# Optimization experiments

Measured on AMD Instinct MI355X. Metric: run time of the kernel, lower is better.

## Reference

```python
import jax, jax.numpy as jnp
import numpy as np

E, S, L, H, C = 32, 64, 20, 512, 32  # episodes, steps, max_comm_len, hidden_size, comm_shape
STD_MIN, STD_MAX = 2.0611536e-09, 7.389056  # exp(-20), exp(2)


def setup_inputs() -> dict:
    key = jax.random.key(0)
    ks = jax.random.split(key, 12)
    def p(k, shape):
        return jax.random.normal(k, shape, jnp.float32) * 0.02
    return {
        'x': jax.random.normal(ks[0], (E, S, H), jnp.float32),
        'Wr': p(ks[1], (2 * H, H)), 'br': jnp.zeros((H,), jnp.float32),
        'Wz': p(ks[2], (2 * H, H)), 'bz': jnp.zeros((H,), jnp.float32),
        'Wn': p(ks[3], (2 * H, H)), 'bn': jnp.zeros((H,), jnp.float32),
        'conv_w1': p(ks[4], (H // 4, H, 1)), 'conv_b1': jnp.zeros((H // 4,), jnp.float32),
        'conv_w3': p(ks[5], (H // 4, H, 3)), 'conv_b3': jnp.zeros((H // 4,), jnp.float32),
        'conv_w5': p(ks[6], (H // 4, H, 5)), 'conv_b5': jnp.zeros((H // 4,), jnp.float32),
        'conv_w7': p(ks[7], (H // 4, H, 7)), 'conv_b7': jnp.zeros((H // 4,), jnp.float32),
        'prelu_a': jnp.asarray(0.25, jnp.float32),
        'W_mu': p(ks[8], (H, C)), 'b_mu': jnp.zeros((C,), jnp.float32),
        'W_std': p(ks[9], (H, C)), 'b_std': jnp.zeros((C,), jnp.float32),
        'eps': jax.random.normal(ks[10], (E, S, L, C), jnp.float32),
    }


def reference(x, Wr, br, Wz, bz, Wn, bn,
              conv_w1, conv_b1, conv_w3, conv_b3, conv_w5, conv_b5, conv_w7, conv_b7,
              prelu_a, W_mu, b_mu, W_std, b_std, eps):
    B = E * S
    xf = x.reshape(B, H)  # same input fed to the RNN at every comm step

    def step(h, _):
        xh = jnp.concatenate([xf, h], -1)
        r = jax.nn.sigmoid(xh @ Wr + br)
        z = jax.nn.sigmoid(xh @ Wz + bz)
        n = jnp.tanh(jnp.concatenate([xf, r * h], -1) @ Wn + bn)
        h_new = (1.0 - z) * n + z * h  # time_constant=1 -> h = new GRU state
        return h_new, h_new

    h0 = jnp.zeros((B, H), x.dtype)
    _, hs = jax.lax.scan(step, h0, None, length=L)  # (L, B, H)
    comm_h = jnp.transpose(hs, (1, 2, 0))  # (B, H, L) -- NCW layout for conv

    dn = ('NCH', 'OIH', 'NCH')
    def conv(w, b, k):
        pad = (k - 1) // 2
        y = jax.lax.conv_general_dilated(comm_h, w, (1,), [(pad, pad)], dimension_numbers=dn)
        return y + b[None, :, None]

    y = jnp.concatenate([
        conv(conv_w1, conv_b1, 1),
        conv(conv_w3, conv_b3, 3),
        conv(conv_w5, conv_b5, 5),
        conv(conv_w7, conv_b7, 7),
    ], axis=1)  # (B, H, L)
    y = jnp.where(y >= 0, y, prelu_a * y)  # PReLU; dropout is identity in eval
    y = jnp.transpose(y, (0, 2, 1)).reshape(E, S, L, H)

    mu = y @ W_mu + b_mu
    std = jnp.clip(jax.nn.softplus(y @ W_std + b_std), STD_MIN, STD_MAX)
    comm = mu + eps * std  # reparameterized Normal sample
    comm_out = jnp.tanh(comm)
    log2pi = jnp.asarray(np.log(2.0 * np.pi), jnp.float32)
    log_prob = (-0.5 * ((comm - mu) / std) ** 2 - jnp.log(std) - 0.5 * log2pi
                - jnp.log(1.0 - comm_out ** 2 + 1e-6))
    log_prob = jnp.mean(log_prob, -1, keepdims=True)  # (E,S,L,1)
    log_prob = jnp.mean(log_prob, -2)  # (E,S,1)
    return comm_out, log_prob
```

## Files before the change

### kernel.cpp

```cpp
#include <hip/hip_runtime.h>
#include <hip/hip_bf16.h>

typedef __hip_bfloat16 bf16;
typedef short short8 __attribute__((ext_vector_type(8)));
typedef float floatx4 __attribute__((ext_vector_type(4)));

#define BDIM 2048
#define HDIM 512
#define LDIM 20
#define CDIM 32
#define LSTR 40

__device__ __forceinline__ float sigm(float x) { return 1.0f / (1.0f + expf(-x)); }

__device__ __forceinline__ void ll16(const short* g, short* l)
{
    __builtin_amdgcn_global_load_lds(
        (const __attribute__((address_space(1))) void*)g,
        (__attribute__((address_space(3))) void*)l, 16, 0, 0);
}
#define WAITVM(N) asm volatile("s_waitcnt vmcnt(" #N ")" ::: "memory")

__device__ __forceinline__ void gemm_tile_k(
    const short* __restrict__ A, int lda,
    const short* __restrict__ Bt, int ldb,
    int K, short* lds, floatx4 (&acc)[4][4], int tid)
{
    short* As = lds;
    short* Bs = lds + 128 * LSTR;
    const int wave = tid >> 6, lane = tid & 63;
    const int wm = wave & 1, wn = wave >> 1;
    const int m16 = lane & 15, quad = lane >> 4;
    const int r0 = tid >> 2;
    const int koff = (tid & 3) * 8;

    short8 a0 = *(const short8*)(A + (size_t)r0 * lda + koff);
    short8 a1 = *(const short8*)(A + (size_t)(r0 + 64) * lda + koff);
    short8 b0 = *(const short8*)(Bt + (size_t)r0 * ldb + koff);
    short8 b1 = *(const short8*)(Bt + (size_t)(r0 + 64) * ldb + koff);
    for (int k0 = 0; k0 < K; k0 += 32) {
        __syncthreads();
        *(short8*)(As + r0 * LSTR + koff) = a0;
        *(short8*)(As + (r0 + 64) * LSTR + koff) = a1;
        *(short8*)(Bs + r0 * LSTR + koff) = b0;
        *(short8*)(Bs + (r0 + 64) * LSTR + koff) = b1;
        __syncthreads();
        if (k0 + 32 < K) {
            a0 = *(const short8*)(A + (size_t)r0 * lda + k0 + 32 + koff);
            a1 = *(const short8*)(A + (size_t)(r0 + 64) * lda + k0 + 32 + koff);
            b0 = *(const short8*)(Bt + (size_t)r0 * ldb + k0 + 32 + koff);
            b1 = *(const short8*)(Bt + (size_t)(r0 + 64) * ldb + k0 + 32 + koff);
        }
        short8 af[4], bfr[4];
#pragma unroll
        for (int i = 0; i < 4; ++i)
            af[i] = *(short8*)(As + (wm * 64 + i * 16 + m16) * LSTR + quad * 8);
#pragma unroll
        for (int j = 0; j < 4; ++j)
            bfr[j] = *(short8*)(Bs + (wn * 64 + j * 16 + m16) * LSTR + quad * 8);
#pragma unroll
        for (int i = 0; i < 4; ++i)
#pragma unroll
            for (int j = 0; j < 4; ++j)
                acc[i][j] = __builtin_amdgcn_mfma_f32_16x16x32_bf16(
                    af[i], bfr[j], acc[i][j], 0, 0, 0);
    }
}

__global__ __launch_bounds__(256) void k_prep_xb(const float* __restrict__ x,
                                                 bf16* __restrict__ xb)
{
    int i = blockIdx.x * 256 + threadIdx.x;
    xb[i] = (bf16)x[i];
}

__global__ __launch_bounds__(256) void k_transpose_512(const float* __restrict__ src,
                                                       bf16* __restrict__ dst)
{
    __shared__ float tile[32][33];
    int tx = threadIdx.x & 31, ty = threadIdx.x >> 5;
    int k0 = blockIdx.x * 32, n0 = blockIdx.y * 32;
#pragma unroll
    for (int i = 0; i < 32; i += 8)
        tile[ty + i][tx] = src[(size_t)(k0 + ty + i) * 512 + n0 + tx];
    __syncthreads();
#pragma unroll
    for (int i = 0; i < 32; i += 8)
        dst[(size_t)(n0 + ty + i) * 512 + k0 + tx] = (bf16)tile[tx][ty + i];
}

__global__ __launch_bounds__(256) void k_swzW(const float* __restrict__ Wr,
                                              const float* __restrict__ Wz,
                                              const float* __restrict__ Wn,
                                              bf16* __restrict__ Wfrag)
{
    int idx = blockIdx.x * 256 + threadIdx.x;
    int e = idx & 7, lane = (idx >> 3) & 63;
    int t2 = idx >> 9;
    int f = t2 % 6, jk = t2 / 6;
    int kc = jk & 15, j = jk >> 4;
    int ftype = f >> 1;
    int col = j * 32 + (f & 1) * 16 + (lane & 15);
    int k = kc * 32 + ((lane >> 4) << 3) + e;
    const float* W = (ftype == 0) ? Wr : (ftype == 1) ? Wz : Wn;
    Wfrag[idx] = (bf16)W[(size_t)(512 + k) * 512 + col];
}

__global__ __launch_bounds__(256) void k_prep_wc(
    const float* __restrict__ w1, const float* __restrict__ w3,
    const float* __restrict__ w5, const float* __restrict__ w7,
    bf16* __restrict__ wt)
{
    int idx = blockIdx.x * 256 + threadIdx.x;
    int g, base;
    if (idx < 65536)       { g = 0; base = 0;      }
    else if (idx < 262144) { g = 1; base = 65536;  }
    else if (idx < 589824) { g = 2; base = 262144; }
    else                   { g = 3; base = 589824; }
    int rel = idx - base;
    int k = 2 * g + 1;
    int ci = rel & 511;
    int t2 = rel >> 9;
    int co = t2 & 127;
    int tap = t2 >> 7;
    const float* w = (g == 0) ? w1 : (g == 1) ? w3 : (g == 2) ? w5 : w7;
    wt[idx] = (bf16)w[((size_t)co * 512 + ci) * k + tap];
}

__global__ __launch_bounds__(256) void k_prep_wh(const float* __restrict__ Wmu,
                                                 const float* __restrict__ Wstd,
                                                 bf16* __restrict__ Wh_t)
{
    int idx = blockIdx.x * 256 + threadIdx.x;
    int n = idx >> 9, k = idx & 511;
    float v = (n < 32) ? Wmu[(size_t)k * 32 + n] : Wstd[(size_t)k * 32 + (n - 32)];
    Wh_t[idx] = (bf16)v;
}

__global__ __launch_bounds__(256) void k_gx(
    const bf16* __restrict__ xb, const bf16* __restrict__ Wx_t,
    const float* __restrict__ br, const float* __restrict__ bz,
    const float* __restrict__ bn, bf16* __restrict__ gxb)
{
    __shared__ short lds[2 * 128 * LSTR];
    const int tid = threadIdx.x;
    const int row0 = blockIdx.x * 128, col0 = blockIdx.y * 128;
    floatx4 acc[4][4];
#pragma unroll
    for (int i = 0; i < 4; ++i)
#pragma unroll
        for (int j = 0; j < 4; ++j) acc[i][j] = (floatx4)0.0f;
    gemm_tile_k((const short*)xb + (size_t)row0 * 512, 512,
                (const short*)Wx_t + (size_t)col0 * 512, 512, 512, lds, acc, tid);
    const int wave = tid >> 6, lane = tid & 63;
    const int wm = wave & 1, wn = wave >> 1;
    const int m16 = lane & 15, quad = lane >> 4;
#pragma unroll
    for (int i = 0; i < 4; ++i)
#pragma unroll
        for (int j = 0; j < 4; ++j)
#pragma unroll
            for (int reg = 0; reg < 4; ++reg) {
                int b = row0 + wm * 64 + i * 16 + quad * 4 + reg;
                int n = col0 + wn * 64 + j * 16 + m16;
                float bias = (n < 512) ? br[n] : (n < 1024) ? bz[n - 512] : bn[n - 1024];
                gxb[(size_t)b * 1536 + n] = (bf16)(acc[i][j][reg] + bias);
            }
}

__device__ __forceinline__ void gbar(unsigned* c, unsigned target, bool fast)
{
    WAITVM(0);
    __syncthreads();
    if (threadIdx.x == 0) {
        if (!fast) __threadfence();
        __hip_atomic_fetch_add(c, 1u, __ATOMIC_RELAXED, __HIP_MEMORY_SCOPE_AGENT);
        unsigned v = __hip_atomic_load(c, __ATOMIC_RELAXED, __HIP_MEMORY_SCOPE_AGENT);
        int guard = 0;
        while (v < target && ++guard < (1 << 24)) {
            __builtin_amdgcn_s_sleep(1);
            v = __hip_atomic_load(c, __ATOMIC_RELAXED, __HIP_MEMORY_SCOPE_AGENT);
        }
        if (!fast) __threadfence();
        else asm volatile("buffer_inv" ::: "memory");
    }
    __syncthreads();
}

template<int NF>
__device__ __forceinline__ void phase_ring(
    const short* __restrict__ srcw, const short* __restrict__ wl,
    short* ringw, int f0, int lane, floatx4 (&acc)[NF])
{
    const short* g = srcw + (size_t)(lane & 15) * 512 + (lane >> 4) * 8;
#pragma unroll
    for (int p = 0; p < 4; ++p)
        ll16(g + p * 32, ringw + p * 512);
#pragma unroll
    for (int kc = 0; kc < 16; ++kc) {
        if (kc < 13)      { WAITVM(3); }
        else if (kc == 13){ WAITVM(2); }
        else if (kc == 14){ WAITVM(1); }
        else              { WAITVM(0); }
        short8 a = *(short8*)(ringw + (kc & 3) * 512 + lane * 8);
        short8 bfr[NF];
#pragma unroll
        for (int f = 0; f < NF; ++f)
            bfr[f] = *(short8*)(wl + ((kc * 6 + f0 + f) << 9) + lane * 8);
        asm volatile("s_waitcnt lgkmcnt(0)" ::: "memory");
        __builtin_amdgcn_sched_barrier(0);
        if (kc < 12)
            ll16(g + (kc + 4) * 32, ringw + (kc & 3) * 512);
#pragma unroll
        for (int f = 0; f < NF; ++f)
            acc[f] = __builtin_amdgcn_mfma_f32_16x16x32_bf16(a, bfr[f], acc[f], 0, 0, 0);
    }
}

__global__ __launch_bounds__(512, 2) void k_gru8(
    const bf16* __restrict__ Wfrag, const bf16* __restrict__ gxb,
    bf16* __restrict__ hs, bf16* __restrict__ rhb,
    unsigned* __restrict__ ctr, int* __restrict__ xcdtab)
{
    __shared__ short wlds[6 * 16 * 512];
    __shared__ short aring[8 * 4 * 512];
    const int tid = threadIdx.x;
    const int wave = tid >> 6, lane = tid & 63;
    const int m16 = lane & 15, quad = lane >> 4;
    const int b = blockIdx.x;
    const int s = b >> 3;
    const int m = (b & 7) + ((s & 1) << 3);
    const int j = s >> 1;
    const int wrow = wave * 16;
    unsigned* mctr = ctr + m * 32;
    short* ringw = aring + wave * 2048;

    int myxcd;
    asm volatile("s_getreg_b32 %0, hwreg(HW_REG_XCC_ID)" : "=s"(myxcd));
    myxcd &= 15;
    if (tid == 0) xcdtab[m * 16 + j] = myxcd;

    const short* wsrc = (const short*)Wfrag + (size_t)j * 49152;
#pragma unroll
    for (int r = 0; r < 12; ++r)
        ll16(wsrc + ((wave * 12 + r) << 9) + lane * 8, wlds + ((wave * 12 + r) << 9));

    float gxr[2][4], gxz[2][4], gxn[2][4];
#pragma unroll
    for (int reg = 0; reg < 4; ++reg) {
        const bf16* gp = gxb + (size_t)(m * 128 + wrow + quad * 4 + reg) * 1536 + j * 32;
#pragma unroll
        for (int fc = 0; fc < 2; ++fc) {
            int c = fc * 16 + m16;
            gxr[fc][reg] = __bfloat162float(gp[c]);
            gxz[fc][reg] = __bfloat162float(gp[512 + c]);
            gxn[fc][reg] = __bfloat162float(gp[1024 + c]);
        }
    }

    gbar(mctr + 1, 16u, false);
    bool fast = true;
#pragma unroll
    for (int jj = 0; jj < 16; ++jj)
        fast = fast && (xcdtab[m * 16 + jj] == myxcd);

    float h32[2][4] = {};
    float zf[2][4];
    unsigned nbar = 0;
    const int rowg = m * 128 + wrow + quad * 4;

    for (int t = 0; t < LDIM; ++t) {
        floatx4 acc[4];
#pragma unroll
        for (int f = 0; f < 4; ++f) acc[f] = (floatx4)0.0f;
        if (t > 0)
            phase_ring<4>((const short*)hs + ((size_t)(t - 1) * BDIM + m * 128 + wrow) * 512,
                          wlds, ringw, 0, lane, acc);
#pragma unroll
        for (int fc = 0; fc < 2; ++fc)
#pragma unroll
            for (int reg = 0; reg < 4; ++reg) {
                float r = sigm(acc[fc][reg] + gxr[fc][reg]);
                zf[fc][reg] = sigm(acc[2 + fc][reg] + gxz[fc][reg]);
                if (t > 0)
                    rhb[(size_t)(rowg + reg) * 512 + j * 32 + fc * 16 + m16] =
                        (bf16)(r * h32[fc][reg]);
            }
        if (t > 0) { ++nbar; gbar(mctr, nbar * 16u, fast); }
        floatx4 acc2[2];
#pragma unroll
        for (int f = 0; f < 2; ++f) acc2[f] = (floatx4)0.0f;
        if (t > 0)
            phase_ring<2>((const short*)rhb + (size_t)(m * 128 + wrow) * 512,
                          wlds, ringw, 4, lane, acc2);
#pragma unroll
        for (int fc = 0; fc < 2; ++fc)
#pragma unroll
            for (int reg = 0; reg < 4; ++reg) {
                float nv = tanhf(acc2[fc][reg] + gxn[fc][reg]);
                float z = zf[fc][reg];
                float hn = (1.0f - z) * nv + z * h32[fc][reg];
                h32[fc][reg] = hn;
                hs[((size_t)t * BDIM + rowg + reg) * 512 + j * 32 + fc * 16 + m16] =
                    (bf16)hn;
            }
        if (t < LDIM - 1) { ++nbar; gbar(mctr, nbar * 16u, fast); }
    }
}

__global__ __launch_bounds__(256) void k_conv(
    const bf16* __restrict__ hs, const bf16* __restrict__ Wc_t,
    const float* __restrict__ b1, const float* __restrict__ b3,
    const float* __restrict__ b5, const float* __restrict__ b7,
    const float* __restrict__ pa, bf16* __restrict__ y)
{
    __shared__ short lds[2 * 128 * LSTR];
    const int tid = threadIdx.x;
    const int btile = blockIdx.x, g = blockIdx.y, l = blockIdx.z;
    const int row0 = btile * 128;
    const int ktap = 2 * g + 1, p = g;
    const int offs[4] = {0, 65536, 262144, 589824};
    const short* Wg = (const short*)Wc_t + offs[g];
    floatx4 acc[4][4];
#pragma unroll
    for (int i = 0; i < 4; ++i)
#pragma unroll
        for (int j = 0; j < 4; ++j) acc[i][j] = (floatx4)0.0f;
    for (int tap = 0; tap < ktap; ++tap) {
        int li = l + tap - p;
        if (li < 0 || li >= LDIM) continue;
        gemm_tile_k((const short*)hs + (size_t)li * BDIM * HDIM + (size_t)row0 * 512, 512,
                    Wg + (size_t)tap * 128 * 512, 512, 512, lds, acc, tid);
    }
    const float* bp = (g == 0) ? b1 : (g == 1) ? b3 : (g == 2) ? b5 : b7;
    const float a = *pa;
    const int wave = tid >> 6, lane = tid & 63;
    const int wm = wave & 1, wn = wave >> 1;
    const int m16 = lane & 15, quad = lane >> 4;
#pragma unroll
    for (int i = 0; i < 4; ++i)
#pragma unroll
        for (int j = 0; j < 4; ++j)
#pragma unroll
            for (int reg = 0; reg < 4; ++reg) {
                int b = row0 + wm * 64 + i * 16 + quad * 4 + reg;
                int col = wn * 64 + j * 16 + m16;
                float v = acc[i][j][reg] + bp[col];
                v = (v >= 0.0f) ? v : a * v;
                y[((size_t)b * LDIM + l) * 512 + g * 128 + col] = (bf16)v;
            }
}

__global__ __launch_bounds__(256) void k_head2(
    const bf16* __restrict__ y, const bf16* __restrict__ Wh_t,
    const float* __restrict__ bmu, const float* __restrict__ bstd,
    const float* __restrict__ eps, float* __restrict__ out_comm,
    float* __restrict__ lpsum)
{
    __shared__ short As[128 * LSTR];
    __shared__ short Bs[64 * LSTR];
    const int tid = threadIdx.x;
    const int wave = tid >> 6, lane = tid & 63;
    const int m16 = lane & 15, quad = lane >> 4;
    const int r0 = tid >> 2, koff = (tid & 3) * 8;
    const int row0 = blockIdx.x * 128;
    floatx4 acc[2][4];
#pragma unroll
    for (int i = 0; i < 2; ++i)
#pragma unroll
        for (int j = 0; j < 4; ++j) acc[i][j] = (floatx4)0.0f;
    const short* Ap = (const short*)y + (size_t)row0 * 512;
    const short* Bp = (const short*)Wh_t;
    short8 ga0 = *(const short8*)(Ap + (size_t)r0 * 512 + koff);
    short8 ga1 = *(const short8*)(Ap + (size_t)(r0 + 64) * 512 + koff);
    short8 gb0 = *(const short8*)(Bp + (size_t)r0 * 512 + koff);
    for (int k0 = 0; k0 < 512; k0 += 32) {
        __syncthreads();
        *(short8*)(As + r0 * LSTR + koff) = ga0;
        *(short8*)(As + (r0 + 64) * LSTR + koff) = ga1;
        *(short8*)(Bs + r0 * LSTR + koff) = gb0;
        __syncthreads();
        if (k0 + 32 < 512) {
            ga0 = *(const short8*)(Ap + (size_t)r0 * 512 + k0 + 32 + koff);
            ga1 = *(const short8*)(Ap + (size_t)(r0 + 64) * 512 + k0 + 32 + koff);
            gb0 = *(const short8*)(Bp + (size_t)r0 * 512 + k0 + 32 + koff);
        }
        short8 af[2], bfr[4];
#pragma unroll
        for (int i = 0; i < 2; ++i)
            af[i] = *(short8*)(As + (wave * 32 + i * 16 + m16) * LSTR + quad * 8);
#pragma unroll
        for (int j = 0; j < 4; ++j)
            bfr[j] = *(short8*)(Bs + (j * 16 + m16) * LSTR + quad * 8);
#pragma unroll
        for (int i = 0; i < 2; ++i)
#pragma unroll
            for (int j = 0; j < 4; ++j)
                acc[i][j] = __builtin_amdgcn_mfma_f32_16x16x32_bf16(
                    af[i], bfr[j], acc[i][j], 0, 0, 0);
    }
#pragma unroll
    for (int i = 0; i < 2; ++i)
#pragma unroll
        for (int reg = 0; reg < 4; ++reg) {
            int row = row0 + wave * 32 + i * 16 + quad * 4 + reg;
            float lp = 0.0f;
#pragma unroll
            for (int jj = 0; jj < 2; ++jj) {
                int c = jj * 16 + m16;
                float mu = acc[i][jj][reg] + bmu[c];
                float sraw = acc[i][jj + 2][reg] + bstd[c];
                float sp = (sraw > 20.0f) ? sraw : log1pf(expf(sraw));
                float sd = fminf(fmaxf(sp, 2.0611536e-09f), 7.389056f);
                float e = eps[(size_t)row * 32 + c];
                float comm = fmaf(e, sd, mu);
                float tt = tanhf(comm);
                out_comm[(size_t)row * 32 + c] = tt;
                lp += -0.5f * e * e - logf(sd) - 0.91893853320467274f
                      - logf(1.0f - tt * tt + 1e-6f);
            }
            lp += __shfl_xor(lp, 1, 16);
            lp += __shfl_xor(lp, 2, 16);
            lp += __shfl_xor(lp, 4, 16);
            lp += __shfl_xor(lp, 8, 16);
            if (m16 == 0) lpsum[row] = lp;
        }
}

__global__ __launch_bounds__(256) void k_final(const float* __restrict__ lpsum,
                                               float* __restrict__ out2)
{
    int b = blockIdx.x * 256 + threadIdx.x;
    if (b < BDIM) {
        float s = 0.0f;
#pragma unroll
        for (int i = 0; i < LDIM; ++i) s += lpsum[b * LDIM + i];
        out2[b] = s * (1.0f / (LDIM * CDIM));
    }
}

extern "C" void kernel_launch(void* const* d_in, const int* in_sizes, int n_in,
                              void* d_out, int out_size, void* d_ws, size_t ws_size,
                              hipStream_t stream)
{
    const float* x    = (const float*)d_in[0];
    const float* Wr   = (const float*)d_in[1];
    const float* br   = (const float*)d_in[2];
    const float* Wz   = (const float*)d_in[3];
    const float* bz   = (const float*)d_in[4];
    const float* Wn   = (const float*)d_in[5];
    const float* bn   = (const float*)d_in[6];
    const float* w1   = (const float*)d_in[7];
    const float* b1   = (const float*)d_in[8];
    const float* w3   = (const float*)d_in[9];
    const float* b3   = (const float*)d_in[10];
    const float* w5   = (const float*)d_in[11];
    const float* b5   = (const float*)d_in[12];
    const float* w7   = (const float*)d_in[13];
    const float* b7   = (const float*)d_in[14];
    const float* pa   = (const float*)d_in[15];
    const float* Wmu  = (const float*)d_in[16];
    const float* bmu  = (const float*)d_in[17];
    const float* Wstd = (const float*)d_in[18];
    const float* bstd = (const float*)d_in[19];
    const float* eps  = (const float*)d_in[20];

    char* cur = (char*)d_ws;
    auto alloc = [&](size_t bytes) -> void* {
        void* r = (void*)cur;
        cur += (bytes + 255) & ~(size_t)255;
        return r;
    };
    const size_t BH = (size_t)BDIM * HDIM;
    bf16*  gxb   = (bf16*)alloc((size_t)BDIM * 1536 * 2);
    bf16*  xb    = (bf16*)alloc(BH * 2);
    bf16*  hs    = (bf16*)alloc(BH * LDIM * 2);
    bf16*  ybuf  = (bf16*)alloc(BH * LDIM * 2);
    bf16*  Wx_t  = (bf16*)alloc((size_t)1536 * 512 * 2);
    bf16*  Wfrag = (bf16*)alloc((size_t)786432 * 2);
    bf16*  Wc_t  = (bf16*)alloc((size_t)1048576 * 2);
    bf16*  Wh_t  = (bf16*)alloc((size_t)64 * 512 * 2);
    bf16*  rhb   = (bf16*)alloc((size_t)BDIM * 512 * 2);
    float* lpsum = (float*)alloc((size_t)BDIM * LDIM * 4);
    unsigned* ctr = (unsigned*)alloc(2048);
    int*   xcdtab = (int*)alloc(1024);

    hipMemsetAsync(ctr, 0, 2048, stream);

    k_prep_xb<<<4096, 256, 0, stream>>>(x, xb);
    dim3 tg(16, 16);
    k_transpose_512<<<tg, 256, 0, stream>>>(Wr, Wx_t);
    k_transpose_512<<<tg, 256, 0, stream>>>(Wz, Wx_t + 262144);
    k_transpose_512<<<tg, 256, 0, stream>>>(Wn, Wx_t + 524288);
    k_swzW<<<3072, 256, 0, stream>>>(Wr, Wz, Wn, Wfrag);
    k_prep_wc<<<4096, 256, 0, stream>>>(w1, w3, w5, w7, Wc_t);
    k_prep_wh<<<128, 256, 0, stream>>>(Wmu, Wstd, Wh_t);

    k_gx<<<dim3(16, 12), 256, 0, stream>>>(xb, Wx_t, br, bz, bn, gxb);

    k_gru8<<<256, 512, 0, stream>>>(Wfrag, gxb, hs, rhb, ctr, xcdtab);

    k_conv<<<dim3(16, 4, 20), 256, 0, stream>>>(hs, Wc_t, b1, b3, b5, b7, pa, ybuf);

    float* out_comm = (float*)d_out;
    float* out_lp   = (float*)d_out + (size_t)BDIM * LDIM * CDIM;
    k_head2<<<320, 256, 0, stream>>>(ybuf, Wh_t, bmu, bstd, eps, out_comm, lpsum);
    k_final<<<8, 256, 0, stream>>>(lpsum, out_lp);
}
```

Before: 529.8 us.

## Rework GRU barrier to per-block flags, register A loads, peel step zero, bigger conv tiles

The GRU grid barrier changes from a single atomic counter, which every block increments and polls, to per-block flag slots that one wave polls in parallel with a ballot. This is meant to cut atomic contention on the recurrent critical path. The LDS ring staging of the h/rh operand is replaced by loading all 16 K-chunks straight into registers, which raises register pressure. The t=0 step is peeled out because h0 is zero, removing one matmul phase and one barrier. The conv kernel moves to 256-row tiles with 512 threads, so each weight tile is reused across twice as many rows.

```diff
diff --git a/kernel.cpp b/kernel.cpp
--- a/kernel.cpp
+++ b/kernel.cpp
@@ -67,6 +67,49 @@
     }
 }
 
+__device__ __forceinline__ void gemm_tile_k256(
+    const short* __restrict__ A,
+    const short* __restrict__ Bt,
+    short* lds, floatx4 (&acc)[4][4], int tid)
+{
+    short* As = lds;
+    short* Bs = lds + 256 * LSTR;
+    const int wave = tid >> 6, lane = tid & 63;
+    const int wm = wave & 3, wn = wave >> 2;
+    const int m16 = lane & 15, quad = lane >> 4;
+    const int r0 = tid >> 2;
+    const int koff = (tid & 3) * 8;
+
+    short8 a0 = *(const short8*)(A + (size_t)r0 * 512 + koff);
+    short8 a1 = *(const short8*)(A + (size_t)(r0 + 128) * 512 + koff);
+    short8 b0 = *(const short8*)(Bt + (size_t)r0 * 512 + koff);
+    for (int k0 = 0; k0 < 512; k0 += 32) {
+        __syncthreads();
+        *(short8*)(As + r0 * LSTR + koff) = a0;
+        *(short8*)(As + (r0 + 128) * LSTR + koff) = a1;
+        *(short8*)(Bs + r0 * LSTR + koff) = b0;
+        __syncthreads();
+        if (k0 + 32 < 512) {
+            a0 = *(const short8*)(A + (size_t)r0 * 512 + k0 + 32 + koff);
+            a1 = *(const short8*)(A + (size_t)(r0 + 128) * 512 + k0 + 32 + koff);
+            b0 = *(const short8*)(Bt + (size_t)r0 * 512 + k0 + 32 + koff);
+        }
+        short8 af[4], bfr[4];
+#pragma unroll
+        for (int i = 0; i < 4; ++i)
+            af[i] = *(short8*)(As + (wm * 64 + i * 16 + m16) * LSTR + quad * 8);
+#pragma unroll
+        for (int j = 0; j < 4; ++j)
+            bfr[j] = *(short8*)(Bs + (wn * 64 + j * 16 + m16) * LSTR + quad * 8);
+#pragma unroll
+        for (int i = 0; i < 4; ++i)
+#pragma unroll
+            for (int j = 0; j < 4; ++j)
+                acc[i][j] = __builtin_amdgcn_mfma_f32_16x16x32_bf16(
+                    af[i], bfr[j], acc[i][j], 0, 0, 0);
+    }
+}
+
 __global__ __launch_bounds__(256) void k_prep_xb(const float* __restrict__ x,
                                                  bf16* __restrict__ xb)
 {
@@ -168,62 +211,58 @@
             }
 }
 
-__device__ __forceinline__ void gbar(unsigned* c, unsigned target, bool fast)
+__device__ __forceinline__ void gbar2(unsigned* flags, int j, unsigned target,
+                                      bool fast, int tid)
 {
     WAITVM(0);
     __syncthreads();
-    if (threadIdx.x == 0) {
-        if (!fast) __threadfence();
-        __hip_atomic_fetch_add(c, 1u, __ATOMIC_RELAXED, __HIP_MEMORY_SCOPE_AGENT);
-        unsigned v = __hip_atomic_load(c, __ATOMIC_RELAXED, __HIP_MEMORY_SCOPE_AGENT);
-        int guard = 0;
-        while (v < target && ++guard < (1 << 24)) {
-            __builtin_amdgcn_s_sleep(1);
-            v = __hip_atomic_load(c, __ATOMIC_RELAXED, __HIP_MEMORY_SCOPE_AGENT);
-        }
-        if (!fast) __threadfence();
+    if (tid < 64) {
+        if (tid == 0) {
+            if (!fast) __threadfence();
+            __hip_atomic_store(flags + j, target, __ATOMIC_RELAXED,
+                               __HIP_MEMORY_SCOPE_AGENT);
+        }
+        unsigned v; int guard = 0;
+        do {
+            v = (tid < 16) ? __hip_atomic_load(flags + tid, __ATOMIC_RELAXED,
+                                               __HIP_MEMORY_SCOPE_AGENT)
+                           : target;
+        } while (__ballot(v >= target) != ~0ull && ++guard < (1 << 20));
+        if (!fast) { if (tid == 0) __threadfence(); }
         else asm volatile("buffer_inv" ::: "memory");
     }
     __syncthreads();
 }
 
 template<int NF>
-__device__ __forceinline__ void phase_ring(
+__device__ __forceinline__ void phase_reg(
     const short* __restrict__ srcw, const short* __restrict__ wl,
-    short* ringw, int f0, int lane, floatx4 (&acc)[NF])
+    int f0, int lane, floatx4 (&acc)[NF])
 {
     const short* g = srcw + (size_t)(lane & 15) * 512 + (lane >> 4) * 8;
-#pragma unroll
-    for (int p = 0; p < 4; ++p)
-        ll16(g + p * 32, ringw + p * 512);
+    short8 a[16];
+#pragma unroll
+    for (int kc = 0; kc < 16; ++kc)
+        a[kc] = *(const short8*)(g + kc * 32);
 #pragma unroll
     for (int kc = 0; kc < 16; ++kc) {
-        if (kc < 13)      { WAITVM(3); }
-        else if (kc == 13){ WAITVM(2); }
-        else if (kc == 14){ WAITVM(1); }
-        else              { WAITVM(0); }
-        short8 a = *(short8*)(ringw + (kc & 3) * 512 + lane * 8);
         short8 bfr[NF];
 #pragma unroll
         for (int f = 0; f < NF; ++f)
             bfr[f] = *(short8*)(wl + ((kc * 6 + f0 + f) << 9) + lane * 8);
-        asm volatile("s_waitcnt lgkmcnt(0)" ::: "memory");
-        __builtin_amdgcn_sched_barrier(0);
-        if (kc < 12)
-            ll16(g + (kc + 4) * 32, ringw + (kc & 3) * 512);
 #pragma unroll
         for (int f = 0; f < NF; ++f)
-            acc[f] = __builtin_amdgcn_mfma_f32_16x16x32_bf16(a, bfr[f], acc[f], 0, 0, 0);
-    }
-}
-
-__global__ __launch_bounds__(512, 2) void k_gru8(
+            acc[f] = __builtin_amdgcn_mfma_f32_16x16x32_bf16(a[kc], bfr[f],
+                                                             acc[f], 0, 0, 0);
+    }
+}
+
+__global__ __launch_bounds__(512, 2) void k_gru9(
     const bf16* __restrict__ Wfrag, const bf16* __restrict__ gxb,
     bf16* __restrict__ hs, bf16* __restrict__ rhb,
     unsigned* __restrict__ ctr, int* __restrict__ xcdtab)
 {
     __shared__ short wlds[6 * 16 * 512];
-    __shared__ short aring[8 * 4 * 512];
     const int tid = threadIdx.x;
     const int wave = tid >> 6, lane = tid & 63;
     const int m16 = lane & 15, quad = lane >> 4;
@@ -232,8 +271,8 @@
     const int m = (b & 7) + ((s & 1) << 3);
     const int j = s >> 1;
     const int wrow = wave * 16;
-    unsigned* mctr = ctr + m * 32;
-    short* ringw = aring + wave * 2048;
+    unsigned* flg  = ctr + m * 32;
+    unsigned* vflg = ctr + m * 32 + 16;
 
     int myxcd;
     asm volatile("s_getreg_b32 %0, hwreg(HW_REG_XCC_ID)" : "=s"(myxcd));
@@ -258,41 +297,53 @@
         }
     }
 
-    gbar(mctr + 1, 16u, false);
+    gbar2(vflg, j, 1u, false, tid);
     bool fast = true;
 #pragma unroll
-    for (int jj = 0; jj < 16; ++jj)
-        fast = fast && (xcdtab[m * 16 + jj] == myxcd);
-
-    float h32[2][4] = {};
+    for (int jj = 0; jj < 16; ++jj) {
+        int xv = __hip_atomic_load((const int*)xcdtab + m * 16 + jj,
+                                   __ATOMIC_RELAXED, __HIP_MEMORY_SCOPE_AGENT);
+        fast = fast && (xv == myxcd);
+    }
+
+    float h32[2][4];
     float zf[2][4];
     unsigned nbar = 0;
     const int rowg = m * 128 + wrow + quad * 4;
 
-    for (int t = 0; t < LDIM; ++t) {
+#pragma unroll
+    for (int fc = 0; fc < 2; ++fc)
+#pragma unroll
+        for (int reg = 0; reg < 4; ++reg) {
+            float z = sigm(gxz[fc][reg]);
+            float nv = tanhf(gxn[fc][reg]);
+            float hn = (1.0f - z) * nv;
+            h32[fc][reg] = hn;
+            hs[(size_t)(rowg + reg) * 512 + j * 32 + fc * 16 + m16] = (bf16)hn;
+        }
+    ++nbar; gbar2(flg, j, nbar, fast, tid);
+
+    for (int t = 1; t < LDIM; ++t) {
         floatx4 acc[4];
 #pragma unroll
         for (int f = 0; f < 4; ++f) acc[f] = (floatx4)0.0f;
-        if (t > 0)
-            phase_ring<4>((const short*)hs + ((size_t)(t - 1) * BDIM + m * 128 + wrow) * 512,
-                          wlds, ringw, 0, lane, acc);
+        phase_reg<4>((const short*)hs + ((size_t)(t - 1) * BDIM + m * 128 + wrow) * 512,
+                     wlds, 0, lane, acc);
 #pragma unroll
         for (int fc = 0; fc < 2; ++fc)
 #pragma unroll
             for (int reg = 0; reg < 4; ++reg) {
                 float r = sigm(acc[fc][reg] + gxr[fc][reg]);
                 zf[fc][reg] = sigm(acc[2 + fc][reg] + gxz[fc][reg]);
-                if (t > 0)
-                    rhb[(size_t)(rowg + reg) * 512 + j * 32 + fc * 16 + m16] =
-                        (bf16)(r * h32[fc][reg]);
+                rhb[(size_t)(rowg + reg) * 512 + j * 32 + fc * 16 + m16] =
+                    (bf16)(r * h32[fc][reg]);
             }
-        if (t > 0) { ++nbar; gbar(mctr, nbar * 16u, fast); }
+        ++nbar; gbar2(flg, j, nbar, fast, tid);
         floatx4 acc2[2];
 #pragma unroll
         for (int f = 0; f < 2; ++f) acc2[f] = (floatx4)0.0f;
-        if (t > 0)
-            phase_ring<2>((const short*)rhb + (size_t)(m * 128 + wrow) * 512,
-                          wlds, ringw, 4, lane, acc2);
+        phase_reg<2>((const short*)rhb + (size_t)(m * 128 + wrow) * 512,
+                     wlds, 4, lane, acc2);
 #pragma unroll
         for (int fc = 0; fc < 2; ++fc)
 #pragma unroll
@@ -304,20 +355,20 @@
                 hs[((size_t)t * BDIM + rowg + reg) * 512 + j * 32 + fc * 16 + m16] =
                     (bf16)hn;
             }
-        if (t < LDIM - 1) { ++nbar; gbar(mctr, nbar * 16u, fast); }
-    }
-}
-
-__global__ __launch_bounds__(256) void k_conv(
+        if (t < LDIM - 1) { ++nbar; gbar2(flg, j, nbar, fast, tid); }
+    }
+}
+
+__global__ __launch_bounds__(512, 2) void k_conv(
     const bf16* __restrict__ hs, const bf16* __restrict__ Wc_t,
     const float* __restrict__ b1, const float* __restrict__ b3,
     const float* __restrict__ b5, const float* __restrict__ b7,
     const float* __restrict__ pa, bf16* __restrict__ y)
 {
-    __shared__ short lds[2 * 128 * LSTR];
+    __shared__ short lds[(256 + 128) * LSTR];
     const int tid = threadIdx.x;
     const int btile = blockIdx.x, g = blockIdx.y, l = blockIdx.z;
-    const int row0 = btile * 128;
+    const int row0 = btile * 256;
     const int ktap = 2 * g + 1, p = g;
     const int offs[4] = {0, 65536, 262144, 589824};
     const short* Wg = (const short*)Wc_t + offs[g];
@@ -329,13 +380,13 @@
     for (int tap = 0; tap < ktap; ++tap) {
         int li = l + tap - p;
         if (li < 0 || li >= LDIM) continue;
-        gemm_tile_k((const short*)hs + (size_t)li * BDIM * HDIM + (size_t)row0 * 512, 512,
-                    Wg + (size_t)tap * 128 * 512, 512, 512, lds, acc, tid);
+        gemm_tile_k256((const short*)hs + (size_t)li * BDIM * HDIM + (size_t)row0 * 512,
+                       Wg + (size_t)tap * 128 * 512, lds, acc, tid);
     }
     const float* bp = (g == 0) ? b1 : (g == 1) ? b3 : (g == 2) ? b5 : b7;
     const float a = *pa;
     const int wave = tid >> 6, lane = tid & 63;
-    const int wm = wave & 1, wn = wave >> 1;
+    const int wm = wave & 3, wn = wave >> 2;
     const int m16 = lane & 15, quad = lane >> 4;
 #pragma unroll
     for (int i = 0; i < 4; ++i)
@@ -498,9 +549,9 @@
 
     k_gx<<<dim3(16, 12), 256, 0, stream>>>(xb, Wx_t, br, bz, bn, gxb);
 
-    k_gru8<<<256, 512, 0, stream>>>(Wfrag, gxb, hs, rhb, ctr, xcdtab);
-
-    k_conv<<<dim3(16, 4, 20), 256, 0, stream>>>(hs, Wc_t, b1, b3, b5, b7, pa, ybuf);
+    k_gru9<<<256, 512, 0, stream>>>(Wfrag, gxb, hs, rhb, ctr, xcdtab);
+
+    k_conv<<<dim3(8, 4, 20), 512, 0, stream>>>(hs, Wc_t, b1, b3, b5, b7, pa, ybuf);
 
     float* out_comm = (float*)d_out;
     float* out_lp   = (float*)d_out + (size_t)BDIM * LDIM * CDIM;
```

Result: no change. 537.9 us (+1.5%).
